# Performance work log

Measured on AMD Instinct MI355X. Metric: run time of the kernel, lower is better.

## Reference

```python
import jax, jax.numpy as jnp
import numpy as np

B, S = 2, 2048          # 2 sequences of length 2048 (prefill, equal-length varlen batch)
H, HKV, D = 32, 1, 64   # query heads, kv heads (MQA), head size
HID = H * D             # 2048
T = B * S
SCALE = D ** -0.5


def setup_inputs() -> dict:
    key = jax.random.key(0)
    k1, k2, k3 = jax.random.split(key, 3)
    hidden_states = jax.random.normal(k1, (T, HID), dtype=jnp.float32)
    # rotary tables: positions restart per sequence, NeoX half-rotation, base 10000
    inv_freq = 1.0 / (10000.0 ** (jnp.arange(0, D, 2, dtype=jnp.float32) / D))  # [D/2]
    pos = jnp.tile(jnp.arange(S, dtype=jnp.float32), B)                          # [T]
    freqs = pos[:, None] * inv_freq[None, :]                                     # [T, D/2]
    cos = jnp.cos(freqs)[:, None, :]                                             # [T,1,D/2]
    sin = jnp.sin(freqs)[:, None, :]
    w_qkv = jax.random.normal(k2, ((H + 2 * HKV) * D, HID), dtype=jnp.float32) * (HID ** -0.5)
    w_dense = jax.random.normal(k3, (HID, H * D), dtype=jnp.float32) * (HID ** -0.5)
    return {"hidden_states": hidden_states, "cos": cos, "sin": sin,
            "w_qkv": w_qkv, "w_dense": w_dense}


def _rope(x, cos, sin):
    # x: [T, nh, D]; cos/sin: [T, 1, D/2]; NeoX-style half rotation
    x1, x2 = x[..., : D // 2], x[..., D // 2:]
    return jnp.concatenate([x1 * cos - x2 * sin, x2 * cos + x1 * sin], axis=-1)


def reference(hidden_states, cos, sin, w_qkv, w_dense):
    qkv = hidden_states @ w_qkv.T                                # [T, (H+2*HKV)*D]
    q, kvf = jnp.split(qkv, [H * D], axis=1)
    q = q.reshape(T, H, D)
    kv = kvf.reshape(T, 2, HKV, D)
    q = _rope(q, cos, sin)
    k = _rope(kv[:, 0], cos, sin)                                # [T, HKV, D]
    v = kv[:, 1]                                                 # [T, HKV, D]
    # varlen prefill attention: reshape to [B,S,...]; MQA broadcast kv over H heads
    qb = q.reshape(B, S, H, D)
    kb = k.reshape(B, S, HKV, D)[:, :, 0, :]                     # [B,S,D]
    vb = v.reshape(B, S, HKV, D)[:, :, 0, :]
    scores = jnp.einsum("bshd,btd->bhst", qb, kb) * SCALE        # [B,H,S,S]
    causal = jnp.tril(jnp.ones((S, S), dtype=bool))
    scores = jnp.where(causal[None, None], scores, jnp.float32(-1e30))
    probs = jax.nn.softmax(scores, axis=-1)
    attn = jnp.einsum("bhst,btd->bshd", probs, vb)               # [B,S,H,D]
    return attn.reshape(T, H * D) @ w_dense.T                    # [T, HID]
```

## Files before the change

kernel.cpp:

```cpp
#include <hip/hip_runtime.h>

#define BB   2
#define SS   2048
#define TT   4096
#define HH   32
#define DD   64
#define HIDN 2048
#define NQKV 2176
#define QK_SCALE_LOG2 0.1803368801f

#define AS1 __attribute__((address_space(1)))
#define AS3 __attribute__((address_space(3)))

typedef __attribute__((ext_vector_type(8))) short short8;
typedef __attribute__((ext_vector_type(4))) float f32x4;
typedef __attribute__((ext_vector_type(16))) float f32x16;
typedef __attribute__((ext_vector_type(4))) unsigned short ushort4_t;
typedef __attribute__((ext_vector_type(4))) unsigned int uint4_t;

__device__ inline unsigned short f2bf(float f) {
  unsigned int u = __builtin_bit_cast(unsigned int, f);
  u += 0x7FFFu + ((u >> 16) & 1u);
  return (unsigned short)(u >> 16);
}
__device__ inline float bf2f(unsigned short s) {
  unsigned int u = ((unsigned int)s) << 16;
  return __builtin_bit_cast(float, u);
}
__device__ inline float exp2fast(float x) { return __builtin_amdgcn_exp2f(x); }

__global__ __launch_bounds__(256)
void cvt_all_kernel(const float* __restrict__ hs, const float* __restrict__ wqkv,
                    const float* __restrict__ wd, unsigned short* __restrict__ out) {
  int i = blockIdx.x * 256 + threadIdx.x;
  if (i >= 4259840) return;
  const float* src; int off;
  if (i < 2097152)      { src = hs;   off = i; }
  else if (i < 3211264) { src = wqkv; off = i - 2097152; }
  else                  { src = wd;   off = i - 3211264; }
  float4 v = ((const float4*)src)[off];
  ushort4_t u = { f2bf(v.x), f2bf(v.y), f2bf(v.z), f2bf(v.w) };
  *(ushort4_t*)(out + (long)i * 4) = u;
}

template<int OUT_BF16>
__global__ __launch_bounds__(256)
void gemm_bt(const unsigned short* __restrict__ A, const unsigned short* __restrict__ Bw,
             void* __restrict__ Cp, int M, int N, int K) {
  __shared__ unsigned char lAB[65536];
  const int tid  = threadIdx.x;
  const int lane = tid & 63;
  const int wv   = tid >> 6;
  const int wr   = wv >> 1, wc = wv & 1;
  const int g    = lane >> 4, qq = lane & 15;
  const int gx   = gridDim.x;
  const int nwg  = gx * gridDim.y;
  const int lid  = blockIdx.y * gx + blockIdx.x;
  const int swz  = (lid & 7) * (nwg >> 3) + (lid >> 3);
  const long bm0 = (long)(swz / gx) * 128;
  const long bn0 = (long)(swz % gx) * 128;
  const int srow  = tid >> 4;
  const int scolu = ((((tid & 15) << 4) ^ ((srow & 15) << 4)) >> 1);

  f32x4 zero = {0.f, 0.f, 0.f, 0.f};
  f32x4 acc[4][4];
#pragma unroll
  for (int m = 0; m < 4; ++m)
#pragma unroll
    for (int n = 0; n < 4; ++n) acc[m][n] = zero;

  const unsigned short* aSrc = A  + (bm0 + srow) * K + scolu;
  const unsigned short* bSrc = Bw + (bn0 + srow) * K + scolu;
  const int rswz = qq << 4;

  for (int k0 = 0; k0 < K; k0 += 128) {
    __syncthreads();
#pragma unroll
    for (int gg = 0; gg < 8; ++gg) {
      __builtin_amdgcn_global_load_lds(
          (const AS1 unsigned int*)(aSrc + k0 + (long)16 * gg * K),
          (AS3 unsigned int*)(lAB + gg * 4096 + wv * 1024), 16, 0, 0);
      __builtin_amdgcn_global_load_lds(
          (const AS1 unsigned int*)(bSrc + k0 + (long)16 * gg * K),
          (AS3 unsigned int*)(lAB + 32768 + gg * 4096 + wv * 1024), 16, 0, 0);
    }
    __syncthreads();

#pragma unroll
    for (int ks = 0; ks < 4; ++ks) {
      short8 af[4], bf[4];
#pragma unroll
      for (int m = 0; m < 4; ++m)
        af[m] = *(const short8*)(lAB + (wr * 64 + m * 16 + qq) * 256
                                     + ((ks * 64 + g * 16) ^ rswz));
#pragma unroll
      for (int n = 0; n < 4; ++n)
        bf[n] = *(const short8*)(lAB + 32768 + (wc * 64 + n * 16 + qq) * 256
                                     + ((ks * 64 + g * 16) ^ rswz));
#pragma unroll
      for (int m = 0; m < 4; ++m)
#pragma unroll
        for (int n = 0; n < 4; ++n)
          acc[m][n] = __builtin_amdgcn_mfma_f32_16x16x32_bf16(af[m], bf[n], acc[m][n], 0, 0, 0);
    }
  }

#pragma unroll
  for (int m = 0; m < 4; ++m) {
#pragma unroll
    for (int r = 0; r < 4; ++r) {
      long row = bm0 + wr * 64 + m * 16 + g * 4 + r;
#pragma unroll
      for (int n = 0; n < 4; ++n) {
        long col = bn0 + wc * 64 + n * 16 + qq;
        float v = acc[m][n][r];
        if (OUT_BF16) ((unsigned short*)Cp)[row * N + col] = f2bf(v);
        else          ((float*)Cp)[row * N + col] = v;
      }
    }
  }
}

__global__ __launch_bounds__(256)
void rope_kernel(const unsigned short* __restrict__ qkv, const float* __restrict__ cosb,
                 const float* __restrict__ sinb, unsigned short* __restrict__ q_out,
                 unsigned short* __restrict__ k_out, unsigned short* __restrict__ v_out) {
  int idx = blockIdx.x * 256 + threadIdx.x;
  if (idx >= TT * 136) return;
  int t   = idx / 136;
  int rem = idx - t * 136;
  int hh  = rem >> 2;
  int i0  = (rem & 3) * 8;
  const unsigned short* row = qkv + (long)t * NQKV;

  if (hh < 33) {
    const unsigned short* src = row + (hh < 32 ? hh * 64 : 2048);
    short8 a = *(const short8*)(src + i0);
    short8 b = *(const short8*)(src + 32 + i0);
    float cv[8], sv[8];
    *(float4*)(cv)     = *(const float4*)(cosb + t * 32 + i0);
    *(float4*)(cv + 4) = *(const float4*)(cosb + t * 32 + i0 + 4);
    *(float4*)(sv)     = *(const float4*)(sinb + t * 32 + i0);
    *(float4*)(sv + 4) = *(const float4*)(sinb + t * 32 + i0 + 4);
    const float sc = (hh < 32) ? QK_SCALE_LOG2 : 1.f;
    short8 ra, rb;
#pragma unroll
    for (int j = 0; j < 8; ++j) {
      float x1 = bf2f((unsigned short)a[j]);
      float x2 = bf2f((unsigned short)b[j]);
      ra[j] = (short)f2bf((x1 * cv[j] - x2 * sv[j]) * sc);
      rb[j] = (short)f2bf((x2 * cv[j] + x1 * sv[j]) * sc);
    }
    unsigned short* dst = (hh < 32) ? q_out + ((long)t * 32 + hh) * 64
                                    : k_out + (long)t * 64;
    *(short8*)(dst + i0)      = ra;
    *(short8*)(dst + 32 + i0) = rb;
  } else {
    const unsigned short* src = row + 2112;
    short8 a = *(const short8*)(src + i0);
    short8 b = *(const short8*)(src + 32 + i0);
    int bb = t >> 11, s = t & 2047;
    int tile = s >> 6, c = s & 63;
    long base = ((long)bb * 32 + tile) * 64;
#pragma unroll
    for (int j = 0; j < 8; ++j) {
      v_out[(base + i0 + j) * 64 + c]      = (unsigned short)a[j];
      v_out[(base + 32 + i0 + j) * 64 + c] = (unsigned short)b[j];
    }
  }
}

__global__ __launch_bounds__(256, 2)
void attn_kernel(const unsigned short* __restrict__ qs, const unsigned short* __restrict__ kr,
                 const unsigned short* __restrict__ vt, unsigned short* __restrict__ ob) {
  __shared__ unsigned char lsm[32768];
  const int tid  = threadIdx.x;
  const int lane = tid & 63;
  const int wv   = tid >> 6;
  const int half = lane >> 5;
  const int qc   = lane & 31;
  const int h    = blockIdx.y * 4 + wv;
  const int b    = blockIdx.z;
  const int qtA  = blockIdx.x;
  const int qtB  = (SS / 32 - 1) - blockIdx.x;
  const int q0A  = qtA * 32, q0B = qtB * 32;
  const int nbA  = (q0A >> 7) + 1, nbB = (q0B >> 7) + 1;

  const unsigned short* kb  = kr + (long)b * SS * 64;
  const unsigned short* vtb = vt + (long)b * (SS / 64) * 64 * 64;

  const int srow = tid >> 3;
  const int scol = ((((tid & 7) << 4) ^ ((srow & 7) << 4)) >> 1);

  const int rswz = (qc & 7) << 4;
  int roff[4];
#pragma unroll
  for (int i = 0; i < 4; ++i)
    roff[i] = qc * 128 + ((i * 32 + half * 16) ^ rswz);

  short8 qfA[4], qfB[4];
  {
    const unsigned short* qrA = qs + ((long)(b * SS + q0A + qc) * HH + h) * 64;
    const unsigned short* qrB = qs + ((long)(b * SS + q0B + qc) * HH + h) * 64;
#pragma unroll
    for (int dstep = 0; dstep < 4; ++dstep) {
      qfA[dstep] = *(const short8*)(qrA + dstep * 16 + half * 8);
      qfB[dstep] = *(const short8*)(qrB + dstep * 16 + half * 8);
    }
  }

  f32x16 oA0, oA1, oB0, oB1;
#pragma unroll
  for (int r = 0; r < 16; ++r) { oA0[r] = 0.f; oA1[r] = 0.f; oB0[r] = 0.f; oB1[r] = 0.f; }
  float mA = -1e30f, lA = 0.f, mB = -1e30f, lB = 0.f;

#define PHASE(qf, o0, o1, mst, lst, q0x, isLast)                                 \
  do {                                                                           \
    f32x16 st0, st1;                                                             \
    _Pragma("unroll")                                                            \
    for (int r = 0; r < 16; ++r) { st0[r] = 0.f; st1[r] = 0.f; }                 \
    __builtin_amdgcn_s_setprio(1);                                               \
    _Pragma("unroll")                                                            \
    for (int dstep = 0; dstep < 4; ++dstep) {                                    \
      short8 kfA_ = *(const short8*)(Kb + roff[dstep]);                          \
      short8 kfB_ = *(const short8*)(Kb + roff[dstep] + 4096);                   \
      st0 = __builtin_amdgcn_mfma_f32_32x32x16_bf16(kfA_, qf[dstep], st0, 0, 0, 0); \
      st1 = __builtin_amdgcn_mfma_f32_32x32x16_bf16(kfB_, qf[dstep], st1, 0, 0, 0); \
    }                                                                            \
    __builtin_amdgcn_s_setprio(0);                                               \
    if (isLast) {                                                                \
      _Pragma("unroll")                                                          \
      for (int r = 0; r < 16; ++r) {                                             \
        int rkv = (r & 3) + 8 * (r >> 2) + 4 * half;                             \
        if (kvb + rkv      > (q0x) + qc) st0[r] = -1e30f;                        \
        if (kvb + 32 + rkv > (q0x) + qc) st1[r] = -1e30f;                        \
      }                                                                          \
    }                                                                            \
    float pmax = st0[0];                                                         \
    _Pragma("unroll")                                                            \
    for (int r = 1; r < 16; ++r) pmax = fmaxf(pmax, st0[r]);                     \
    _Pragma("unroll")                                                            \
    for (int r = 0; r < 16; ++r) pmax = fmaxf(pmax, st1[r]);                     \
    pmax = fmaxf(pmax, __shfl_xor(pmax, 32));                                    \
    if (!__all(pmax - mst <= 8.f)) {                                             \
      const float mnew = fmaxf(mst, pmax);                                       \
      const float scal = exp2fast(mst - mnew);                                   \
      lst *= scal;                                                               \
      _Pragma("unroll")                                                          \
      for (int r = 0; r < 16; ++r) { o0[r] *= scal; o1[r] *= scal; }             \
      mst = mnew;                                                                \
    }                                                                            \
    float psum = 0.f;                                                            \
    _Pragma("unroll")                                                            \
    for (int r = 0; r < 16; ++r) { st0[r] = exp2fast(st0[r] - mst); psum += st0[r]; } \
    _Pragma("unroll")                                                            \
    for (int r = 0; r < 16; ++r) { st1[r] = exp2fast(st1[r] - mst); psum += st1[r]; } \
    psum += __shfl_xor(psum, 32);                                                \
    lst += psum;                                                                 \
    short8 pb[4];                                                                \
    _Pragma("unroll")                                                            \
    for (int hseg = 0; hseg < 2; ++hseg) {                                       \
      const f32x16& pp = hseg ? st1 : st0;                                       \
      unsigned int a0, a1, a2, a3, a4, a5, a6, a7;                               \
      asm("v_cvt_pk_bf16_f32 %0, %1, %2" : "=v"(a0) : "v"(pp[0]),  "v"(pp[1]));  \
      asm("v_cvt_pk_bf16_f32 %0, %1, %2" : "=v"(a1) : "v"(pp[2]),  "v"(pp[3]));  \
      asm("v_cvt_pk_bf16_f32 %0, %1, %2" : "=v"(a2) : "v"(pp[4]),  "v"(pp[5]));  \
      asm("v_cvt_pk_bf16_f32 %0, %1, %2" : "=v"(a3) : "v"(pp[6]),  "v"(pp[7]));  \
      asm("v_cvt_pk_bf16_f32 %0, %1, %2" : "=v"(a4) : "v"(pp[8]),  "v"(pp[9]));  \
      asm("v_cvt_pk_bf16_f32 %0, %1, %2" : "=v"(a5) : "v"(pp[10]), "v"(pp[11])); \
      asm("v_cvt_pk_bf16_f32 %0, %1, %2" : "=v"(a6) : "v"(pp[12]), "v"(pp[13])); \
      asm("v_cvt_pk_bf16_f32 %0, %1, %2" : "=v"(a7) : "v"(pp[14]), "v"(pp[15])); \
      asm("v_permlane32_swap_b32 %0, %1" : "+v"(a0), "+v"(a2));                  \
      asm("v_permlane32_swap_b32 %0, %1" : "+v"(a1), "+v"(a3));                  \
      asm("v_permlane32_swap_b32 %0, %1" : "+v"(a4), "+v"(a6));                  \
      asm("v_permlane32_swap_b32 %0, %1" : "+v"(a5), "+v"(a7));                  \
      uint4_t w0 = { a0, a1, a2, a3 };                                           \
      uint4_t w1 = { a4, a5, a6, a7 };                                           \
      pb[hseg * 2]     = __builtin_bit_cast(short8, w0);                         \
      pb[hseg * 2 + 1] = __builtin_bit_cast(short8, w1);                         \
    }                                                                            \
    __builtin_amdgcn_s_setprio(1);                                               \
    _Pragma("unroll")                                                            \
    for (int ks = 0; ks < 4; ++ks) {                                             \
      short8 vfA_ = *(const short8*)(Vb + roff[ks]);                             \
      short8 vfB_ = *(const short8*)(Vb + roff[ks] + 4096);                      \
      o0 = __builtin_amdgcn_mfma_f32_32x32x16_bf16(vfA_, pb[ks], o0, 0, 0, 0);   \
      o1 = __builtin_amdgcn_mfma_f32_32x32x16_bf16(vfB_, pb[ks], o1, 0, 0, 0);   \
    }                                                                            \
    __builtin_amdgcn_s_setprio(0);                                               \
  } while (0)

  for (int ib = 0; ib < nbB; ++ib) {
    const int kv0 = ib * 128;
    __syncthreads();
    {
      const unsigned short* kS = kb + ((long)(kv0 + srow)) * 64 + scol;
#pragma unroll
      for (int gg = 0; gg < 4; ++gg)
        __builtin_amdgcn_global_load_lds((const AS1 unsigned int*)(kS + gg * 32 * 64),
            (AS3 unsigned int*)(lsm + gg * 4096 + wv * 1024), 16, 0, 0);
      const unsigned short* vS = vtb + (long)(2 * ib) * 4096 + srow * 64 + scol;
#pragma unroll
      for (int gg = 0; gg < 4; ++gg)
        __builtin_amdgcn_global_load_lds((const AS1 unsigned int*)(vS + gg * 32 * 64),
            (AS3 unsigned int*)(lsm + 16384 + gg * 4096 + wv * 1024), 16, 0, 0);
    }
    __syncthreads();

    for (int ph = 0; ph < 2; ++ph) {
      const unsigned char* Kb = lsm + ph * 8192;
      const unsigned char* Vb = lsm + 16384 + ph * 8192;
      const int kvb = kv0 + ph * 64;
      if (!(ph && ib == nbB - 1 && (q0B & 127) < 64))
        PHASE(qfB, oB0, oB1, mB, lB, q0B, ib == nbB - 1);
      if (ib < nbA && !(ph && ib == nbA - 1 && (q0A & 127) < 64))
        PHASE(qfA, oA0, oA1, mA, lA, q0A, ib == nbA - 1);
    }
  }
#undef PHASE

  {
    const float inv = 1.f / lA;
    unsigned short* orow = ob + ((long)(b * SS + q0A + qc) * HH + h) * 64;
#pragma unroll
    for (int r = 0; r < 16; ++r) {
      int d0 = (r & 3) + 8 * (r >> 2) + 4 * half;
      orow[d0]      = f2bf(oA0[r] * inv);
      orow[32 + d0] = f2bf(oA1[r] * inv);
    }
  }
  {
    const float inv = 1.f / lB;
    unsigned short* orow = ob + ((long)(b * SS + q0B + qc) * HH + h) * 64;
#pragma unroll
    for (int r = 0; r < 16; ++r) {
      int d0 = (r & 3) + 8 * (r >> 2) + 4 * half;
      orow[d0]      = f2bf(oB0[r] * inv);
      orow[32 + d0] = f2bf(oB1[r] * inv);
    }
  }
}

extern "C" void kernel_launch(void* const* d_in, const int* in_sizes, int n_in,
                              void* d_out, int out_size, void* d_ws, size_t ws_size,
                              hipStream_t stream) {
  const float* hs   = (const float*)d_in[0];
  const float* cosb = (const float*)d_in[1];
  const float* sinb = (const float*)d_in[2];
  const float* wqkv = (const float*)d_in[3];
  const float* wd   = (const float*)d_in[4];

  char* ws = (char*)d_ws;
  unsigned short* hs_bf   = (unsigned short*)(ws);
  unsigned short* wqkv_bf = (unsigned short*)(ws + 16777216);
  unsigned short* wd_bf   = (unsigned short*)(ws + 25690112);
  unsigned short* qkv_bf  = (unsigned short*)(ws + 34078720);
  unsigned short* q_bf    = (unsigned short*)(ws + 51904512);
  unsigned short* k_bf    = (unsigned short*)(ws + 68681728);
  unsigned short* vt_bf   = (unsigned short*)(ws + 69206016);

  cvt_all_kernel<<<16640, 256, 0, stream>>>(hs, wqkv, wd, hs_bf);

  gemm_bt<1><<<dim3(17, 32), 256, 0, stream>>>(hs_bf, wqkv_bf, qkv_bf, TT, NQKV, HIDN);

  rope_kernel<<<2176, 256, 0, stream>>>(qkv_bf, cosb, sinb, q_bf, k_bf, vt_bf);

  attn_kernel<<<dim3(SS / 64, 8, BB), 256, 0, stream>>>(q_bf, k_bf, vt_bf, hs_bf);

  gemm_bt<0><<<dim3(16, 32), 256, 0, stream>>>(hs_bf, wd_bf, d_out, TT, HIDN, HIDN);
}
```

Baseline: 182.5 us.

## Split-K the KV columns of the QKV GEMM to balance waves and fuse reduction into rope

```diff
diff --git a/kernel.cpp b/kernel.cpp
--- a/kernel.cpp
+++ b/kernel.cpp
@@ -43,10 +43,106 @@
   *(ushort4_t*)(out + (long)i * 4) = u;
 }
 
-template<int OUT_BF16>
 __global__ __launch_bounds__(256)
-void gemm_bt(const unsigned short* __restrict__ A, const unsigned short* __restrict__ Bw,
-             void* __restrict__ Cp, int M, int N, int K) {
+void gemm_qkv_split(const unsigned short* __restrict__ A, const unsigned short* __restrict__ Bw,
+                    unsigned short* __restrict__ qout, float* __restrict__ kvp) {
+  __shared__ unsigned char lAB[65536];
+  const int K = HIDN;
+  const int tid  = threadIdx.x;
+  const int lane = tid & 63;
+  const int wv   = tid >> 6;
+  const int wr   = wv >> 1, wc = wv & 1;
+  const int g    = lane >> 4, qq = lane & 15;
+
+  long bm0, bn0; int kbeg, kend, isQ = 0, ks = 0;
+  const int bid = blockIdx.x;
+  if (bid < 512) {
+    const int swz = (bid & 7) * 64 + (bid >> 3);
+    isQ = 1;
+    bm0 = (long)(swz >> 4) * 128;
+    bn0 = (long)(swz & 15) * 128;
+    kbeg = 0; kend = 2048;
+  } else {
+    const int r = bid - 512;
+    bm0 = (long)(r >> 1) * 128;
+    bn0 = 2048;
+    ks  = r & 1;
+    kbeg = ks * 1024; kend = kbeg + 1024;
+  }
+
+  const int srow  = tid >> 4;
+  const int scolu = ((((tid & 15) << 4) ^ ((srow & 15) << 4)) >> 1);
+
+  f32x4 zero = {0.f, 0.f, 0.f, 0.f};
+  f32x4 acc[4][4];
+#pragma unroll
+  for (int m = 0; m < 4; ++m)
+#pragma unroll
+    for (int n = 0; n < 4; ++n) acc[m][n] = zero;
+
+  const unsigned short* aSrc = A  + (bm0 + srow) * K + scolu;
+  const unsigned short* bSrc = Bw + (bn0 + srow) * K + scolu;
+  const int rswz = qq << 4;
+
+  for (int k0 = kbeg; k0 < kend; k0 += 128) {
+    __syncthreads();
+#pragma unroll
+    for (int gg = 0; gg < 8; ++gg) {
+      __builtin_amdgcn_global_load_lds(
+          (const AS1 unsigned int*)(aSrc + k0 + (long)16 * gg * K),
+          (AS3 unsigned int*)(lAB + gg * 4096 + wv * 1024), 16, 0, 0);
+      __builtin_amdgcn_global_load_lds(
+          (const AS1 unsigned int*)(bSrc + k0 + (long)16 * gg * K),
+          (AS3 unsigned int*)(lAB + 32768 + gg * 4096 + wv * 1024), 16, 0, 0);
+    }
+    __syncthreads();
+
+#pragma unroll
+    for (int kss = 0; kss < 4; ++kss) {
+      short8 af[4], bf[4];
+#pragma unroll
+      for (int m = 0; m < 4; ++m)
+        af[m] = *(const short8*)(lAB + (wr * 64 + m * 16 + qq) * 256
+                                     + ((kss * 64 + g * 16) ^ rswz));
+#pragma unroll
+      for (int n = 0; n < 4; ++n)
+        bf[n] = *(const short8*)(lAB + 32768 + (wc * 64 + n * 16 + qq) * 256
+                                     + ((kss * 64 + g * 16) ^ rswz));
+#pragma unroll
+      for (int m = 0; m < 4; ++m)
+#pragma unroll
+        for (int n = 0; n < 4; ++n)
+          acc[m][n] = __builtin_amdgcn_mfma_f32_16x16x32_bf16(af[m], bf[n], acc[m][n], 0, 0, 0);
+    }
+  }
+
+  if (isQ) {
+#pragma unroll
+    for (int m = 0; m < 4; ++m)
+#pragma unroll
+      for (int r = 0; r < 4; ++r) {
+        long row = bm0 + wr * 64 + m * 16 + g * 4 + r;
+#pragma unroll
+        for (int n = 0; n < 4; ++n)
+          qout[row * 2048 + bn0 + wc * 64 + n * 16 + qq] = f2bf(acc[m][n][r]);
+      }
+  } else {
+    float* dst = kvp + (long)ks * (4096 * 128);
+#pragma unroll
+    for (int m = 0; m < 4; ++m)
+#pragma unroll
+      for (int r = 0; r < 4; ++r) {
+        long row = bm0 + wr * 64 + m * 16 + g * 4 + r;
+#pragma unroll
+        for (int n = 0; n < 4; ++n)
+          dst[row * 128 + wc * 64 + n * 16 + qq] = acc[m][n][r];
+      }
+  }
+}
+
+__global__ __launch_bounds__(256)
+void gemm_dense(const unsigned short* __restrict__ A, const unsigned short* __restrict__ Bw,
+                float* __restrict__ Cp, int M, int N, int K) {
   __shared__ unsigned char lAB[65536];
   const int tid  = threadIdx.x;
   const int lane = tid & 63;
@@ -87,16 +183,16 @@
     __syncthreads();
 
 #pragma unroll
-    for (int ks = 0; ks < 4; ++ks) {
+    for (int kss = 0; kss < 4; ++kss) {
       short8 af[4], bf[4];
 #pragma unroll
       for (int m = 0; m < 4; ++m)
         af[m] = *(const short8*)(lAB + (wr * 64 + m * 16 + qq) * 256
-                                     + ((ks * 64 + g * 16) ^ rswz));
+                                     + ((kss * 64 + g * 16) ^ rswz));
 #pragma unroll
       for (int n = 0; n < 4; ++n)
         bf[n] = *(const short8*)(lAB + 32768 + (wc * 64 + n * 16 + qq) * 256
-                                     + ((ks * 64 + g * 16) ^ rswz));
+                                     + ((kss * 64 + g * 16) ^ rswz));
 #pragma unroll
       for (int m = 0; m < 4; ++m)
 #pragma unroll
@@ -106,24 +202,19 @@
   }
 
 #pragma unroll
-  for (int m = 0; m < 4; ++m) {
+  for (int m = 0; m < 4; ++m)
 #pragma unroll
     for (int r = 0; r < 4; ++r) {
       long row = bm0 + wr * 64 + m * 16 + g * 4 + r;
 #pragma unroll
-      for (int n = 0; n < 4; ++n) {
-        long col = bn0 + wc * 64 + n * 16 + qq;
-        float v = acc[m][n][r];
-        if (OUT_BF16) ((unsigned short*)Cp)[row * N + col] = f2bf(v);
-        else          ((float*)Cp)[row * N + col] = v;
-      }
-    }
-  }
+      for (int n = 0; n < 4; ++n)
+        Cp[row * N + bn0 + wc * 64 + n * 16 + qq] = acc[m][n][r];
+    }
 }
 
 __global__ __launch_bounds__(256)
-void rope_kernel(const unsigned short* __restrict__ qkv, const float* __restrict__ cosb,
-                 const float* __restrict__ sinb, unsigned short* __restrict__ q_out,
+void rope_kernel(unsigned short* __restrict__ q, const float* __restrict__ kvp,
+                 const float* __restrict__ cosb, const float* __restrict__ sinb,
                  unsigned short* __restrict__ k_out, unsigned short* __restrict__ v_out) {
   int idx = blockIdx.x * 256 + threadIdx.x;
   if (idx >= TT * 136) return;
@@ -131,10 +222,9 @@
   int rem = idx - t * 136;
   int hh  = rem >> 2;
   int i0  = (rem & 3) * 8;
-  const unsigned short* row = qkv + (long)t * NQKV;
-
-  if (hh < 33) {
-    const unsigned short* src = row + (hh < 32 ? hh * 64 : 2048);
+
+  if (hh < 32) {
+    unsigned short* src = q + (long)t * 2048 + hh * 64;
     short8 a = *(const short8*)(src + i0);
     short8 b = *(const short8*)(src + 32 + i0);
     float cv[8], sv[8];
@@ -142,30 +232,42 @@
     *(float4*)(cv + 4) = *(const float4*)(cosb + t * 32 + i0 + 4);
     *(float4*)(sv)     = *(const float4*)(sinb + t * 32 + i0);
     *(float4*)(sv + 4) = *(const float4*)(sinb + t * 32 + i0 + 4);
-    const float sc = (hh < 32) ? QK_SCALE_LOG2 : 1.f;
     short8 ra, rb;
 #pragma unroll
     for (int j = 0; j < 8; ++j) {
       float x1 = bf2f((unsigned short)a[j]);
       float x2 = bf2f((unsigned short)b[j]);
-      ra[j] = (short)f2bf((x1 * cv[j] - x2 * sv[j]) * sc);
-      rb[j] = (short)f2bf((x2 * cv[j] + x1 * sv[j]) * sc);
-    }
-    unsigned short* dst = (hh < 32) ? q_out + ((long)t * 32 + hh) * 64
-                                    : k_out + (long)t * 64;
-    *(short8*)(dst + i0)      = ra;
-    *(short8*)(dst + 32 + i0) = rb;
+      ra[j] = (short)f2bf((x1 * cv[j] - x2 * sv[j]) * QK_SCALE_LOG2);
+      rb[j] = (short)f2bf((x2 * cv[j] + x1 * sv[j]) * QK_SCALE_LOG2);
+    }
+    *(short8*)(src + i0)      = ra;
+    *(short8*)(src + 32 + i0) = rb;
   } else {
-    const unsigned short* src = row + 2112;
-    short8 a = *(const short8*)(src + i0);
-    short8 b = *(const short8*)(src + 32 + i0);
-    int bb = t >> 11, s = t & 2047;
-    int tile = s >> 6, c = s & 63;
-    long base = ((long)bb * 32 + tile) * 64;
-#pragma unroll
-    for (int j = 0; j < 8; ++j) {
-      v_out[(base + i0 + j) * 64 + c]      = (unsigned short)a[j];
-      v_out[(base + 32 + i0 + j) * 64 + c] = (unsigned short)b[j];
+    const float* p0 = kvp + (long)t * 128;
+    const float* p1 = kvp + 4096 * 128 + (long)t * 128;
+    if (hh == 32) {
+      float cv[8], sv[8];
+      *(float4*)(cv)     = *(const float4*)(cosb + t * 32 + i0);
+      *(float4*)(cv + 4) = *(const float4*)(cosb + t * 32 + i0 + 4);
+      *(float4*)(sv)     = *(const float4*)(sinb + t * 32 + i0);
+      *(float4*)(sv + 4) = *(const float4*)(sinb + t * 32 + i0 + 4);
+      unsigned short* kr2 = k_out + (long)t * 64;
+#pragma unroll
+      for (int j = 0; j < 8; ++j) {
+        float x1 = p0[i0 + j]      + p1[i0 + j];
+        float x2 = p0[32 + i0 + j] + p1[32 + i0 + j];
+        kr2[i0 + j]      = f2bf(x1 * cv[j] - x2 * sv[j]);
+        kr2[32 + i0 + j] = f2bf(x2 * cv[j] + x1 * sv[j]);
+      }
+    } else {
+      int bb = t >> 11, s = t & 2047;
+      int tile = s >> 6, c = s & 63;
+      long base = ((long)bb * 32 + tile) * 64;
+#pragma unroll
+      for (int j = 0; j < 8; ++j) {
+        v_out[(base + i0 + j) * 64 + c]      = f2bf(p0[64 + i0 + j] + p1[64 + i0 + j]);
+        v_out[(base + 32 + i0 + j) * 64 + c] = f2bf(p0[96 + i0 + j] + p1[96 + i0 + j]);
+      }
     }
   }
 }
@@ -281,11 +383,11 @@
     }                                                                            \
     __builtin_amdgcn_s_setprio(1);                                               \
     _Pragma("unroll")                                                            \
-    for (int ks = 0; ks < 4; ++ks) {                                             \
-      short8 vfA_ = *(const short8*)(Vb + roff[ks]);                             \
-      short8 vfB_ = *(const short8*)(Vb + roff[ks] + 4096);                      \
-      o0 = __builtin_amdgcn_mfma_f32_32x32x16_bf16(vfA_, pb[ks], o0, 0, 0, 0);   \
-      o1 = __builtin_amdgcn_mfma_f32_32x32x16_bf16(vfB_, pb[ks], o1, 0, 0, 0);   \
+    for (int kss = 0; kss < 4; ++kss) {                                          \
+      short8 vfA_ = *(const short8*)(Vb + roff[kss]);                            \
+      short8 vfB_ = *(const short8*)(Vb + roff[kss] + 4096);                     \
+      o0 = __builtin_amdgcn_mfma_f32_32x32x16_bf16(vfA_, pb[kss], o0, 0, 0, 0);  \
+      o1 = __builtin_amdgcn_mfma_f32_32x32x16_bf16(vfB_, pb[kss], o1, 0, 0, 0);  \
     }                                                                            \
     __builtin_amdgcn_s_setprio(0);                                               \
   } while (0)
@@ -354,18 +456,19 @@
   unsigned short* hs_bf   = (unsigned short*)(ws);
   unsigned short* wqkv_bf = (unsigned short*)(ws + 16777216);
   unsigned short* wd_bf   = (unsigned short*)(ws + 25690112);
-  unsigned short* qkv_bf  = (unsigned short*)(ws + 34078720);
-  unsigned short* q_bf    = (unsigned short*)(ws + 51904512);
-  unsigned short* k_bf    = (unsigned short*)(ws + 68681728);
-  unsigned short* vt_bf   = (unsigned short*)(ws + 69206016);
+  unsigned short* q_bf    = (unsigned short*)(ws + 34078720);
+  float*          kvp     = (float*)(ws + 50855936);
+  unsigned short* k_bf    = (unsigned short*)(ws + 55050240);
+  unsigned short* vt_bf   = (unsigned short*)(ws + 55574528);
 
   cvt_all_kernel<<<16640, 256, 0, stream>>>(hs, wqkv, wd, hs_bf);
 
-  gemm_bt<1><<<dim3(17, 32), 256, 0, stream>>>(hs_bf, wqkv_bf, qkv_bf, TT, NQKV, HIDN);
-
-  rope_kernel<<<2176, 256, 0, stream>>>(qkv_bf, cosb, sinb, q_bf, k_bf, vt_bf);
+  gemm_qkv_split<<<576, 256, 0, stream>>>(hs_bf, wqkv_bf, q_bf, kvp);
+
+  rope_kernel<<<2176, 256, 0, stream>>>(q_bf, kvp, cosb, sinb, k_bf, vt_bf);
 
   attn_kernel<<<dim3(SS / 64, 8, BB), 256, 0, stream>>>(q_bf, k_bf, vt_bf, hs_bf);
 
-  gemm_bt<0><<<dim3(16, 32), 256, 0, stream>>>(hs_bf, wd_bf, d_out, TT, HIDN, HIDN);
-}
+  gemm_dense<<<dim3(16, 32), 256, 0, stream>>>(hs_bf, wd_bf, (float*)d_out,
+                                               TT, HIDN, HIDN);
+}
```

Result: faster. 173.8 us (-4.8%).
